# Kernel tuning notes

Measured on AMD Instinct MI355X. Metric: run time of the kernel, lower is better.

Reference implementation:

```python
import jax, jax.numpy as jnp
import numpy as np

HEAD_NUM = 16
QKV_DIM = 32
EMB = 512
SQRT_EMB = 22.627416997969522  # sqrt(512)
LOGIT_CLIP = 10.0
BATCH, POMO, PROBLEM = 32, 256, 1024


def setup_inputs() -> dict:
    key = jax.random.key(0)
    ks = jax.random.split(key, 8)
    s = 0.02
    return {
        "encoded_nodes": jax.random.normal(ks[0], (BATCH, PROBLEM, EMB), jnp.float32),
        "encoded_q1": jax.random.normal(ks[1], (BATCH, POMO, EMB), jnp.float32),
        "encoded_last_node": jax.random.normal(ks[2], (BATCH, POMO, EMB), jnp.float32),
        "ninf_mask": jnp.zeros((BATCH, POMO, PROBLEM), jnp.float32),
        # weights stored [in, out] so y = x @ W (equiv. to torch Linear with W.T)
        "Wq_first": jax.random.normal(ks[3], (EMB, HEAD_NUM * QKV_DIM), jnp.float32) * s,
        "Wq_last": jax.random.normal(ks[4], (EMB, HEAD_NUM * QKV_DIM), jnp.float32) * s,
        "Wk": jax.random.normal(ks[5], (EMB, HEAD_NUM * QKV_DIM), jnp.float32) * s,
        "Wv": jax.random.normal(ks[6], (EMB, HEAD_NUM * QKV_DIM), jnp.float32) * s,
        "W_combine": jax.random.normal(ks[7], (HEAD_NUM * QKV_DIM, EMB), jnp.float32) * s,
        "b_combine": jnp.zeros((EMB,), jnp.float32),
    }


def _heads(x):
    # [b, n, h*d] -> [b, h, n, d]
    b, n, _ = x.shape
    return x.reshape(b, n, HEAD_NUM, QKV_DIM).transpose(0, 2, 1, 3)


def reference(encoded_nodes, encoded_q1, encoded_last_node, ninf_mask,
              Wq_first, Wq_last, Wk, Wv, W_combine, b_combine):
    # set_kv
    k = _heads(encoded_nodes @ Wk)                     # [b,h,problem,d]
    v = _heads(encoded_nodes @ Wv)                     # [b,h,problem,d]
    single_head_key = encoded_nodes.transpose(0, 2, 1) # [b,emb,problem]
    # set_q1
    q_first = _heads(encoded_q1 @ Wq_first)            # [b,h,pomo,d]
    # forward
    q_last = _heads(encoded_last_node @ Wq_last)       # [b,h,pomo,d]
    q = q_first + q_last

    scale = 1.0 / jnp.sqrt(jnp.asarray(QKV_DIM, q.dtype))
    score = jnp.einsum("bhnd,bhmd->bhnm", q, k) * scale  # [b,h,pomo,problem]
    score = score + ninf_mask[:, None, :, :]
    weights = jax.nn.softmax(score, axis=-1)
    out = jnp.einsum("bhnm,bhmd->bhnd", weights, v)      # [b,h,pomo,d]
    out_concat = out.transpose(0, 2, 1, 3).reshape(q.shape[0], q.shape[2], HEAD_NUM * QKV_DIM)
    mh_out = out_concat @ W_combine + b_combine          # [b,pomo,emb]

    score2 = jnp.einsum("bne,bem->bnm", mh_out, single_head_key) / SQRT_EMB
    score2 = LOGIT_CLIP * jnp.tanh(score2) + ninf_mask
    probs = jax.nn.softmax(score2, axis=2)               # [b,pomo,problem]
    return probs
```

## Files before the change

kernel.cpp:

```cpp
#include <hip/hip_runtime.h>
#include <math.h>

typedef unsigned short u16;
typedef __attribute__((ext_vector_type(8))) short bf16x8;
typedef __attribute__((ext_vector_type(4))) float f32x4;
typedef __attribute__((ext_vector_type(4))) int i32x4;
typedef __attribute__((ext_vector_type(4))) short s16x4;
typedef __attribute__((ext_vector_type(4))) unsigned short u16x4;

#define MFMA16(a,b,c) __builtin_amdgcn_mfma_f32_16x16x32_bf16((a),(b),(c),0,0,0)

__device__ __forceinline__ u16 f2bf(float x){
  unsigned int u = __float_as_uint(x);
  u += 0x7fffu + ((u >> 16) & 1u);
  return (u16)(u >> 16);
}
__device__ __forceinline__ float bf2f(u16 x){
  return __uint_as_float(((unsigned)x) << 16);
}
__device__ __forceinline__ void gload16(const void* g, void* l){
  __builtin_amdgcn_global_load_lds((const __attribute__((address_space(1))) void*)g,
                                   (__attribute__((address_space(3))) void*)l, 16, 0, 0);
}

__global__ __launch_bounds__(256) void prep(
    const float* __restrict__ nodes, const float* __restrict__ q1, const float* __restrict__ lastn,
    const float* __restrict__ mask,
    const float* __restrict__ Wqf, const float* __restrict__ Wql, const float* __restrict__ Wk,
    const float* __restrict__ Wv, const float* __restrict__ Wc,
    u16* __restrict__ nodesb, u16* __restrict__ q1b, u16* __restrict__ lastb,
    u16* __restrict__ WtKV, u16* __restrict__ WtQF, u16* __restrict__ WtQL, u16* __restrict__ WtC,
    u16* __restrict__ maskP)
{
  const int tid = blockIdx.x * 256 + threadIdx.x;
  const int NT = 1048576;
  for (int i = tid; i < 4194304; i += NT) {
    float4 v = ((const float4*)nodes)[i];
    u16x4 o; o[0]=f2bf(v.x); o[1]=f2bf(v.y); o[2]=f2bf(v.z); o[3]=f2bf(v.w);
    *(u16x4*)&nodesb[i*4] = o;
  }
  {
    float4 v = ((const float4*)q1)[tid];
    u16x4 o; o[0]=f2bf(v.x); o[1]=f2bf(v.y); o[2]=f2bf(v.z); o[3]=f2bf(v.w);
    *(u16x4*)&q1b[tid*4] = o;
    v = ((const float4*)lastn)[tid];
    o[0]=f2bf(v.x); o[1]=f2bf(v.y); o[2]=f2bf(v.z); o[3]=f2bf(v.w);
    *(u16x4*)&lastb[tid*4] = o;
  }
  if (tid < 262144) {
    int n = tid >> 9, k = tid & 511;
    WtQF[tid] = f2bf(Wqf[k*512 + n]);
    WtQL[tid] = f2bf(Wql[k*512 + n]);
    WtC[tid]  = f2bf(Wc[k*512 + n]);
  }
  if (tid < 524288) {
    int n = tid >> 9, k = tid & 511;
    WtKV[tid] = f2bf(n < 512 ? Wk[k*512 + n] : Wv[k*512 + (n-512)]);
  }
  if (tid < 524288) {
    int brt = tid >> 10, c = tid & 1023;
    const float* mp = mask + (brt*16)*1024 + c;
    u16 vals[16];
    #pragma unroll
    for (int p=0;p<16;p++) vals[p] = f2bf(mp[p*1024]);
    *(i32x4*)&maskP[tid*16]     = *(i32x4*)&vals[0];
    *(i32x4*)&maskP[tid*16 + 8] = *(i32x4*)&vals[8];
  }
}

__global__ __launch_bounds__(256) void gemm_kv(const u16* __restrict__ A, const u16* __restrict__ Bw,
                                               u16* __restrict__ Kout, u16* __restrict__ Vout)
{
  const int mb = (blockIdx.x >> 6)*8 + (blockIdx.x & 7);
  const int nb = (blockIdx.x >> 3) & 7;
  const int t = threadIdx.x, w = t >> 6, l = t & 63, q = l >> 4, ln = l & 15;
  const int wm = (w >> 1) * 64, wn = (w & 1) * 64;
  __shared__ u16 smem[17920];
  f32x4 acc[4][4];
  #pragma unroll
  for (int i=0;i<4;i++)
    #pragma unroll
    for (int j=0;j<4;j++)
      #pragma unroll
      for (int r=0;r<4;r++) acc[i][j][r] = 0.f;
  const int m0 = mb*128, n0 = nb*128;

  #define STAGE_KV(kc_, b_) { \
    u16* sa = smem + (b_)*8192; \
    u16* sb = sa + 4096; \
    _Pragma("unroll") \
    for (int c=0;c<2;c++){ \
      int chunk = c*256 + t; \
      int ko = chunk >> 7, r_ = chunk & 127; \
      gload16(&A[(m0+r_)*512 + (kc_)*32 + ko*8], &sa[chunk*8]); \
      gload16(&Bw[(n0+r_)*512 + (kc_)*32 + ko*8], &sb[chunk*8]); \
    } }

  STAGE_KV(0, 0);
  for (int kc = 0; kc < 16; kc++) {
    __syncthreads();
    if (kc < 15) STAGE_KV(kc+1, (kc+1)&1);
    const u16* sa = smem + (kc&1)*8192;
    const u16* sb = sa + 4096;
    bf16x8 af[4], bfr[4];
    #pragma unroll
    for (int i=0;i<4;i++) af[i] = *(bf16x8*)&sa[(q*128 + wm + i*16 + ln)*8];
    #pragma unroll
    for (int j=0;j<4;j++) bfr[j] = *(bf16x8*)&sb[(q*128 + wn + j*16 + ln)*8];
    #pragma unroll
    for (int i=0;i<4;i++)
      #pragma unroll
      for (int j=0;j<4;j++)
        acc[i][j] = MFMA16(af[i], bfr[j], acc[i][j]);
  }
  #undef STAGE_KV

  __syncthreads();
  #pragma unroll
  for (int i=0;i<4;i++) {
    #pragma unroll
    for (int j=0;j<4;j++) {
      s16x4 o;
      #pragma unroll
      for (int r=0;r<4;r++) o[r] = (short)f2bf(acc[i][j][r]);
      *(s16x4*)&smem[(wn + j*16 + ln)*140 + wm + i*16 + q*4] = o;
    }
  }
  __syncthreads();
  const int bb_ = mb >> 3, mloc = (mb & 7)*128;
  if (nb < 4) {
    u16* base = Kout + ((bb_*16 + nb*4 + w)*1024 + mloc)*32;
    #pragma unroll
    for (int it=0; it<8; it++) {
      int idx = it*512 + l*8;
      int m_ = idx >> 5, d0 = idx & 31;
      int col = w*32 + d0;
      u16 v[8];
      #pragma unroll
      for (int dd=0;dd<8;dd++) v[dd] = smem[(col+dd)*140 + m_];
      *(i32x4*)&base[idx] = *(i32x4*)&v[0];
    }
  } else {
    u16* base = Vout + (((bb_*16 + (nb-4)*4 + w)*32))*1024 + mloc;
    #pragma unroll
    for (int it=0; it<8; it++) {
      int d_ = it*4 + (l >> 4);
      int mc_ = (l & 15)*8;
      *(i32x4*)&base[d_*1024 + mc_] = *(i32x4*)&smem[(w*32 + d_)*140 + mc_];
    }
  }
}

__global__ __launch_bounds__(256) void gemm_q(const u16* __restrict__ A1, const u16* __restrict__ A2,
                                              const u16* __restrict__ B1, const u16* __restrict__ B2,
                                              u16* __restrict__ Qout)
{
  const int mb = (blockIdx.x >> 6)*8 + (blockIdx.x & 7);
  const int nb = (blockIdx.x >> 3) & 7;
  const int t = threadIdx.x, w = t >> 6, l = t & 63, q = l >> 4, ln = l & 15;
  const int wm = (w >> 1) * 32, wn = (w & 1) * 32;
  __shared__ u16 As[4096];
  __shared__ u16 Bs[4096];
  f32x4 acc[2][2];
  #pragma unroll
  for (int i=0;i<2;i++)
    #pragma unroll
    for (int j=0;j<2;j++)
      #pragma unroll
      for (int r=0;r<4;r++) acc[i][j][r] = 0.f;
  const int m0 = mb*64, n0 = nb*64;
  for (int kc = 0; kc < 16; kc++) {
    const u16* Ap = (kc < 8) ? A1 : A2;
    const u16* Bp = (kc < 8) ? B1 : B2;
    const int k0 = (kc & 7) * 64;
    __syncthreads();
    #pragma unroll
    for (int c=0;c<2;c++) {
      int chunk = t + 256*c;
      int row = chunk & 63, ko = chunk >> 6;
      gload16(&Ap[(m0+row)*512 + k0 + ko*8], &As[chunk*8]);
      gload16(&Bp[(n0+row)*512 + k0 + ko*8], &Bs[chunk*8]);
    }
    __syncthreads();
    #pragma unroll
    for (int ko=0;ko<2;ko++) {
      bf16x8 af[2], bfr[2];
      #pragma unroll
      for (int i=0;i<2;i++) af[i] = *(bf16x8*)&As[((ko*4+q)*64 + wm + i*16 + ln)*8];
      #pragma unroll
      for (int j=0;j<2;j++) bfr[j] = *(bf16x8*)&Bs[((ko*4+q)*64 + wn + j*16 + ln)*8];
      #pragma unroll
      for (int i=0;i<2;i++)
        #pragma unroll
        for (int j=0;j<2;j++)
          acc[i][j] = MFMA16(af[i], bfr[j], acc[i][j]);
    }
  }
  const float sc = 0.17677669529663687f;
  #pragma unroll
  for (int i=0;i<2;i++) {
    int gm = m0 + wm + i*16 + q*4;
    int bb = gm >> 8, pm = gm & 255;
    #pragma unroll
    for (int j=0;j<2;j++) {
      int gn = n0 + wn + j*16 + ln;
      int h = gn >> 5, d = gn & 31;
      u16* qp = Qout + ((bb*16 + h)*256 + pm)*32 + d;
      #pragma unroll
      for (int r=0;r<4;r++) qp[r*32] = f2bf(acc[i][j][r]*sc);
    }
  }
}

__global__ __launch_bounds__(256) void attn(const u16* __restrict__ Qg, const u16* __restrict__ Kg,
                                            const u16* __restrict__ Vtg, const u16* __restrict__ maskP,
                                            u16* __restrict__ Og)
{
  const int bid = blockIdx.x;
  const int bh = (bid >> 5)*8 + (bid & 7);
  const int pt = (bid >> 3) & 3;
  const int h = bh & 15, bb = bh >> 4;
  const int t = threadIdx.x, w = t >> 6, l = t & 63, q = l >> 4, ln = l & 15;
  __shared__ u16 Qs[2048];
  __shared__ u16 Ks[4096];
  __shared__ u16 Vs[4096];
  __shared__ u16 Ps[4*640];
  u16* Pw = &Ps[w*640];
  const int qbase = ((bb*16 + h)*256 + pt*64)*32;
  gload16(&Qg[qbase + (t & 63)*32 + (t >> 6)*8], &Qs[t*8]);
  const int kbase = (bb*16 + h)*1024*32;
  const int vbase = (bb*16 + h)*32*1024;
  float rs[4] = {0.f,0.f,0.f,0.f};
  f32x4 oacc[2];
  #pragma unroll
  for (int dt=0;dt<2;dt++)
    #pragma unroll
    for (int r=0;r<4;r++) oacc[dt][r] = 0.f;
  __syncthreads();
  const bf16x8 aq = *(bf16x8*)&Qs[(q*64 + w*16 + ln)*8];
  const u16* mrow = maskP + (bb*16 + pt*4 + w)*16384 + q*4;
  for (int mc = 0; mc < 8; mc++) {
    __syncthreads();
    gload16(&Kg[kbase + (mc*128 + (t & 127))*32 + (t >> 7)*8],       &Ks[t*8]);
    gload16(&Kg[kbase + (mc*128 + (t & 127))*32 + ((t >> 7)+2)*8],   &Ks[(t+256)*8]);
    gload16(&Vtg[vbase + (t & 31)*1024 + mc*128 + (t >> 5)*8],       &Vs[t*8]);
    gload16(&Vtg[vbase + (t & 31)*1024 + mc*128 + ((t >> 5)+8)*8],   &Vs[(t+256)*8]);
    u16x4 mq[8];
    #pragma unroll
    for (int j2=0;j2<8;j2++)
      mq[j2] = *(const u16x4*)&mrow[(mc*128 + j2*16 + ln)*16];
    __syncthreads();
    #pragma unroll
    for (int ch=0; ch<4; ch++) {
      bf16x8 bk0 = *(bf16x8*)&Ks[(q*128 + (ch*2+0)*16 + ln)*8];
      bf16x8 bk1 = *(bf16x8*)&Ks[(q*128 + (ch*2+1)*16 + ln)*8];
      f32x4 zz = {0.f,0.f,0.f,0.f};
      f32x4 s0 = MFMA16(aq, bk0, zz);
      f32x4 s1 = MFMA16(aq, bk1, zz);
      #pragma unroll
      for (int r=0;r<4;r++) {
        float e0 = __expf(s0[r] + bf2f(mq[ch*2+0][r]));
        float e1 = __expf(s1[r] + bf2f(mq[ch*2+1][r]));
        rs[r] += e0 + e1;
        Pw[(q*4+r)*40 + ln]      = f2bf(e0);
        Pw[(q*4+r)*40 + 16 + ln] = f2bf(e1);
      }
      bf16x8 ap  = *(bf16x8*)&Pw[ln*40 + q*8];
      bf16x8 bv0 = *(bf16x8*)&Vs[((ch*4+q)*32 + ln)*8];
      bf16x8 bv1 = *(bf16x8*)&Vs[((ch*4+q)*32 + 16 + ln)*8];
      oacc[0] = MFMA16(ap, bv0, oacc[0]);
      oacc[1] = MFMA16(ap, bv1, oacc[1]);
    }
  }
  #pragma unroll
  for (int r=0;r<4;r++) {
    float v = rs[r];
    v += __shfl_xor(v,1); v += __shfl_xor(v,2); v += __shfl_xor(v,4); v += __shfl_xor(v,8);
    rs[r] = __builtin_amdgcn_rcpf(v);
  }
  const int orow = bb*256 + pt*64 + w*16 + q*4;
  #pragma unroll
  for (int dt=0;dt<2;dt++)
    #pragma unroll
    for (int r=0;r<4;r++)
      Og[(orow + r)*512 + h*32 + dt*16 + ln] = f2bf(oacc[dt][r]*rs[r]);
}

__global__ __launch_bounds__(1024) void cmbfin(const u16* __restrict__ oc, const u16* __restrict__ WtC,
                                               const float* __restrict__ bias,
                                               const u16* __restrict__ nodesb, const u16* __restrict__ maskP,
                                               float* __restrict__ out)
{
  const int bid = blockIdx.x;
  const int bb = bid & 31, rg = bid >> 5;
  const int t = threadIdx.x, w = t >> 6, l = t & 63, q = l >> 4, ln = l & 15;
  __shared__ u16 As[16384];
  __shared__ u16 Ms[16384];
  __shared__ float rsL[16][32];
  const int abase = (bb*256 + rg*32)*512;
  #pragma unroll
  for (int c=0;c<2;c++) {
    int chunk = t + 1024*c;
    gload16(&oc[abase + (chunk & 31)*512 + (chunk >> 5)*8], &As[chunk*8]);
  }
  __syncthreads();
  f32x4 acc1[2][2];
  #pragma unroll
  for (int i=0;i<2;i++)
    #pragma unroll
    for (int ct=0;ct<2;ct++)
      #pragma unroll
      for (int r=0;r<4;r++) acc1[i][ct][r] = 0.f;
  for (int kc=0;kc<16;kc++) {
    bf16x8 af[2];
    #pragma unroll
    for (int i=0;i<2;i++) af[i] = *(bf16x8*)&As[((kc*4 + q)*32 + i*16 + ln)*8];
    #pragma unroll
    for (int ct=0;ct<2;ct++) {
      int col = w*32 + ct*16 + ln;
      bf16x8 bfr = *(const bf16x8*)&WtC[col*512 + kc*32 + q*8];
      #pragma unroll
      for (int i=0;i<2;i++) acc1[i][ct] = MFMA16(af[i], bfr, acc1[i][ct]);
    }
  }
  #pragma unroll
  for (int ct=0;ct<2;ct++) {
    int gn = w*32 + ct*16 + ln;
    float bv = bias[gn];
    #pragma unroll
    for (int i=0;i<2;i++)
      #pragma unroll
      for (int r=0;r<4;r++)
        Ms[(gn >> 3)*256 + (i*16 + q*4 + r)*8 + (gn & 7)] = f2bf(acc1[i][ct][r] + bv);
  }
  __syncthreads();
  float rloc[2][4] = {{0.f,0.f,0.f,0.f},{0.f,0.f,0.f,0.f}};
  const int nbase = bb*524288;
  f32x4 acc[2][4];
  #pragma unroll
  for (int i=0;i<2;i++)
    #pragma unroll
    for (int ct=0;ct<4;ct++)
      #pragma unroll
      for (int r=0;r<4;r++) acc[i][ct][r] = 0.f;
  for (int kc=0;kc<16;kc++) {
    bf16x8 af[2];
    #pragma unroll
    for (int i=0;i<2;i++) af[i] = *(bf16x8*)&Ms[((kc*4 + q)*32 + i*16 + ln)*8];
    #pragma unroll
    for (int ct=0;ct<4;ct++) {
      int col = w*64 + ct*16 + ln;
      bf16x8 bfr = *(const bf16x8*)&nodesb[nbase + col*512 + kc*32 + q*8];
      #pragma unroll
      for (int i=0;i<2;i++) acc[i][ct] = MFMA16(af[i], bfr, acc[i][ct]);
    }
  }
  const float c2 = 0.08838834764831843f;
  const int prow_base = bb*256 + rg*32;
  #pragma unroll
  for (int i=0;i<2;i++) {
    #pragma unroll
    for (int ct=0;ct<4;ct++) {
      int col0 = w*64 + ct*16 + ln;
      u16x4 mv = *(const u16x4*)&maskP[((bb*16 + rg*2 + i)*1024 + col0)*16 + q*4];
      #pragma unroll
      for (int r=0;r<4;r++) {
        float x = acc[i][ct][r] * c2;
        x = fminf(fmaxf(x, -30.f), 30.f);
        float e2 = __expf(x);
        float lg = 10.f*(e2 - 1.f)*__builtin_amdgcn_rcpf(e2 + 1.f) + bf2f(mv[r]);
        float e = __expf(lg);
        rloc[i][r] += e;
        acc[i][ct][r] = e;
      }
    }
  }
  #pragma unroll
  for (int i=0;i<2;i++)
    #pragma unroll
    for (int r=0;r<4;r++) {
      float v = rloc[i][r];
      v += __shfl_xor(v,1); v += __shfl_xor(v,2); v += __shfl_xor(v,4); v += __shfl_xor(v,8);
      rloc[i][r] = v;
    }
  if (ln == 0) {
    #pragma unroll
    for (int i=0;i<2;i++)
      #pragma unroll
      for (int r=0;r<4;r++) rsL[w][i*16 + q*4 + r] = rloc[i][r];
  }
  __syncthreads();
  float inv[2][4];
  #pragma unroll
  for (int i=0;i<2;i++)
    #pragma unroll
    for (int r=0;r<4;r++) {
      float tot = 0.f;
      #pragma unroll
      for (int ww=0;ww<16;ww++) tot += rsL[ww][i*16 + q*4 + r];
      inv[i][r] = __builtin_amdgcn_rcpf(tot);
    }
  #pragma unroll
  for (int i=0;i<2;i++)
    #pragma unroll
    for (int ct=0;ct<4;ct++) {
      int col0 = w*64 + ct*16 + ln;
      #pragma unroll
      for (int r=0;r<4;r++)
        out[(prow_base + i*16 + q*4 + r)*1024 + col0] = acc[i][ct][r]*inv[i][r];
    }
}

extern "C" void kernel_launch(void* const* d_in, const int* in_sizes, int n_in,
                              void* d_out, int out_size, void* d_ws, size_t ws_size,
                              hipStream_t stream)
{
  (void)in_sizes; (void)n_in; (void)out_size; (void)ws_size;
  const float* nodes = (const float*)d_in[0];
  const float* q1    = (const float*)d_in[1];
  const float* lastn = (const float*)d_in[2];
  const float* mask  = (const float*)d_in[3];
  const float* Wqf   = (const float*)d_in[4];
  const float* Wql   = (const float*)d_in[5];
  const float* Wk    = (const float*)d_in[6];
  const float* Wv    = (const float*)d_in[7];
  const float* Wc    = (const float*)d_in[8];
  const float* bias  = (const float*)d_in[9];
  float* out = (float*)d_out;

  char* p = (char*)d_ws;
  u16* nodesb = (u16*)p; p += 33554432;
  u16* q1b    = (u16*)p; p += 8388608;
  u16* lastb  = (u16*)p; p += 8388608;
  u16* WtKV   = (u16*)p; p += 1048576;
  u16* WtQF   = (u16*)p; p += 524288;
  u16* WtQL   = (u16*)p; p += 524288;
  u16* WtC    = (u16*)p; p += 524288;
  u16* Kt     = (u16*)p; p += 33554432;
  u16* Vt     = (u16*)p; p += 33554432;
  u16* Qh     = (u16*)p; p += 8388608;
  u16* maskP  = (u16*)p; p += 16777216;
  u16* oc  = lastb;

  prep<<<4096, 256, 0, stream>>>(nodes, q1, lastn, mask, Wqf, Wql, Wk, Wv, Wc,
                                 nodesb, q1b, lastb, WtKV, WtQF, WtQL, WtC, maskP);
  gemm_kv<<<2048, 256, 0, stream>>>(nodesb, WtKV, Kt, Vt);
  gemm_q<<<1024, 256, 0, stream>>>(q1b, lastb, WtQF, WtQL, Qh);
  attn<<<2048, 256, 0, stream>>>(Qh, Kt, Vt, maskP, oc);
  cmbfin<<<256, 1024, 0, stream>>>(oc, WtC, bias, nodesb, maskP, out);
}
```

Baseline: 396.8 us.

## Fuse K/V and Q projection GEMMs into one 512-thread kernel launch

```diff
diff --git a/kernel.cpp b/kernel.cpp
--- a/kernel.cpp
+++ b/kernel.cpp
@@ -28,8 +28,8 @@
     const float* __restrict__ mask,
     const float* __restrict__ Wqf, const float* __restrict__ Wql, const float* __restrict__ Wk,
     const float* __restrict__ Wv, const float* __restrict__ Wc,
-    u16* __restrict__ nodesb, u16* __restrict__ q1b, u16* __restrict__ lastb,
-    u16* __restrict__ WtKV, u16* __restrict__ WtQF, u16* __restrict__ WtQL, u16* __restrict__ WtC,
+    u16* __restrict__ nodesb, u16* __restrict__ qlb,
+    u16* __restrict__ WtKV, u16* __restrict__ WtQ2, u16* __restrict__ WtC,
     u16* __restrict__ maskP)
 {
   const int tid = blockIdx.x * 256 + threadIdx.x;
@@ -40,17 +40,18 @@
     *(u16x4*)&nodesb[i*4] = o;
   }
   {
+    const int m = tid >> 7, k4 = (tid & 127)*4;
     float4 v = ((const float4*)q1)[tid];
     u16x4 o; o[0]=f2bf(v.x); o[1]=f2bf(v.y); o[2]=f2bf(v.z); o[3]=f2bf(v.w);
-    *(u16x4*)&q1b[tid*4] = o;
+    *(u16x4*)&qlb[m*1024 + k4] = o;
     v = ((const float4*)lastn)[tid];
     o[0]=f2bf(v.x); o[1]=f2bf(v.y); o[2]=f2bf(v.z); o[3]=f2bf(v.w);
-    *(u16x4*)&lastb[tid*4] = o;
+    *(u16x4*)&qlb[m*1024 + 512 + k4] = o;
   }
   if (tid < 262144) {
     int n = tid >> 9, k = tid & 511;
-    WtQF[tid] = f2bf(Wqf[k*512 + n]);
-    WtQL[tid] = f2bf(Wql[k*512 + n]);
+    WtQ2[n*1024 + k]       = f2bf(Wqf[k*512 + n]);
+    WtQ2[n*1024 + 512 + k] = f2bf(Wql[k*512 + n]);
     WtC[tid]  = f2bf(Wc[k*512 + n]);
   }
   if (tid < 524288) {
@@ -68,146 +69,107 @@
   }
 }
 
-__global__ __launch_bounds__(256) void gemm_kv(const u16* __restrict__ A, const u16* __restrict__ Bw,
-                                               u16* __restrict__ Kout, u16* __restrict__ Vout)
+__global__ __launch_bounds__(512, 8) void kvq(
+    const u16* __restrict__ Akv, const u16* __restrict__ Bkv,
+    const u16* __restrict__ Aq,  const u16* __restrict__ Bq,
+    u16* __restrict__ Kout, u16* __restrict__ Vout, u16* __restrict__ Qout)
 {
-  const int mb = (blockIdx.x >> 6)*8 + (blockIdx.x & 7);
-  const int nb = (blockIdx.x >> 3) & 7;
+  __shared__ u16 smem[16384];
   const int t = threadIdx.x, w = t >> 6, l = t & 63, q = l >> 4, ln = l & 15;
-  const int wm = (w >> 1) * 64, wn = (w & 1) * 64;
-  __shared__ u16 smem[17920];
-  f32x4 acc[4][4];
+  const int wc = w & 3;
+  const int wm = (w >> 2) * 64, wn = wc * 32;
+
+  const bool isq = blockIdx.x < 256;
+  int mb, nb, ksteps, kstr;
+  const u16 *Ab, *Bb;
+  if (isq) {
+    const int bid = blockIdx.x;
+    mb = bid >> 2; nb = bid & 3;
+    ksteps = 32; kstr = 1024; Ab = Aq; Bb = Bq;
+  } else {
+    const int bid = blockIdx.x - 256;
+    mb = (bid >> 6)*8 + (bid & 7);
+    nb = (bid >> 3) & 7;
+    ksteps = 16; kstr = 512; Ab = Akv; Bb = Bkv;
+  }
+  const int m0 = mb*128, n0 = nb*128;
+
+  f32x4 acc[4][2];
   #pragma unroll
   for (int i=0;i<4;i++)
     #pragma unroll
-    for (int j=0;j<4;j++)
+    for (int j=0;j<2;j++)
       #pragma unroll
       for (int r=0;r<4;r++) acc[i][j][r] = 0.f;
-  const int m0 = mb*128, n0 = nb*128;
-
-  #define STAGE_KV(kc_, b_) { \
-    u16* sa = smem + (b_)*8192; \
-    u16* sb = sa + 4096; \
-    _Pragma("unroll") \
-    for (int c=0;c<2;c++){ \
-      int chunk = c*256 + t; \
-      int ko = chunk >> 7, r_ = chunk & 127; \
-      gload16(&A[(m0+r_)*512 + (kc_)*32 + ko*8], &sa[chunk*8]); \
-      gload16(&Bw[(n0+r_)*512 + (kc_)*32 + ko*8], &sb[chunk*8]); \
-    } }
-
-  STAGE_KV(0, 0);
-  for (int kc = 0; kc < 16; kc++) {
+
+  const int r_ = t & 127, ko = t >> 7;
+  const u16* Aaddr = Ab + (m0 + r_)*kstr + ko*8;
+  const u16* Baddr = Bb + (n0 + r_)*kstr + ko*8;
+
+  #define STAGE(kc_, b_) { \
+    u16* s = smem + (b_)*8192; \
+    gload16(Aaddr + (kc_)*32, &s[t*8]); \
+    gload16(Baddr + (kc_)*32, &s[4096 + t*8]); }
+
+  STAGE(0, 0);
+  #pragma unroll 2
+  for (int kc = 0; kc < ksteps; kc++) {
     __syncthreads();
-    if (kc < 15) STAGE_KV(kc+1, (kc+1)&1);
+    if (kc + 1 < ksteps) STAGE(kc+1, (kc+1)&1);
     const u16* sa = smem + (kc&1)*8192;
     const u16* sb = sa + 4096;
-    bf16x8 af[4], bfr[4];
-    #pragma unroll
-    for (int i=0;i<4;i++) af[i] = *(bf16x8*)&sa[(q*128 + wm + i*16 + ln)*8];
-    #pragma unroll
-    for (int j=0;j<4;j++) bfr[j] = *(bf16x8*)&sb[(q*128 + wn + j*16 + ln)*8];
-    #pragma unroll
-    for (int i=0;i<4;i++)
-      #pragma unroll
-      for (int j=0;j<4;j++)
-        acc[i][j] = MFMA16(af[i], bfr[j], acc[i][j]);
-  }
-  #undef STAGE_KV
-
-  __syncthreads();
-  #pragma unroll
-  for (int i=0;i<4;i++) {
-    #pragma unroll
-    for (int j=0;j<4;j++) {
-      s16x4 o;
-      #pragma unroll
-      for (int r=0;r<4;r++) o[r] = (short)f2bf(acc[i][j][r]);
-      *(s16x4*)&smem[(wn + j*16 + ln)*140 + wm + i*16 + q*4] = o;
-    }
-  }
-  __syncthreads();
+    bf16x8 bfr[2];
+    #pragma unroll
+    for (int j=0;j<2;j++) bfr[j] = *(bf16x8*)&sb[(q*128 + wn + j*16 + ln)*8];
+    #pragma unroll
+    for (int i=0;i<4;i++) {
+      bf16x8 af = *(bf16x8*)&sa[(q*128 + wm + i*16 + ln)*8];
+      #pragma unroll
+      for (int j=0;j<2;j++)
+        acc[i][j] = MFMA16(af, bfr[j], acc[i][j]);
+    }
+  }
+  #undef STAGE
+
+  const float scale = isq ? 0.17677669529663687f : 1.0f;
   const int bb_ = mb >> 3, mloc = (mb & 7)*128;
-  if (nb < 4) {
-    u16* base = Kout + ((bb_*16 + nb*4 + w)*1024 + mloc)*32;
-    #pragma unroll
-    for (int it=0; it<8; it++) {
-      int idx = it*512 + l*8;
-      int m_ = idx >> 5, d0 = idx & 31;
-      int col = w*32 + d0;
-      u16 v[8];
-      #pragma unroll
-      for (int dd=0;dd<8;dd++) v[dd] = smem[(col+dd)*140 + m_];
-      *(i32x4*)&base[idx] = *(i32x4*)&v[0];
-    }
-  } else {
-    u16* base = Vout + (((bb_*16 + (nb-4)*4 + w)*32))*1024 + mloc;
-    #pragma unroll
-    for (int it=0; it<8; it++) {
-      int d_ = it*4 + (l >> 4);
-      int mc_ = (l & 15)*8;
-      *(i32x4*)&base[d_*1024 + mc_] = *(i32x4*)&smem[(w*32 + d_)*140 + mc_];
-    }
-  }
-}
-
-__global__ __launch_bounds__(256) void gemm_q(const u16* __restrict__ A1, const u16* __restrict__ A2,
-                                              const u16* __restrict__ B1, const u16* __restrict__ B2,
-                                              u16* __restrict__ Qout)
-{
-  const int mb = (blockIdx.x >> 6)*8 + (blockIdx.x & 7);
-  const int nb = (blockIdx.x >> 3) & 7;
-  const int t = threadIdx.x, w = t >> 6, l = t & 63, q = l >> 4, ln = l & 15;
-  const int wm = (w >> 1) * 32, wn = (w & 1) * 32;
-  __shared__ u16 As[4096];
-  __shared__ u16 Bs[4096];
-  f32x4 acc[2][2];
-  #pragma unroll
-  for (int i=0;i<2;i++)
-    #pragma unroll
-    for (int j=0;j<2;j++)
-      #pragma unroll
-      for (int r=0;r<4;r++) acc[i][j][r] = 0.f;
-  const int m0 = mb*64, n0 = nb*64;
-  for (int kc = 0; kc < 16; kc++) {
-    const u16* Ap = (kc < 8) ? A1 : A2;
-    const u16* Bp = (kc < 8) ? B1 : B2;
-    const int k0 = (kc & 7) * 64;
+  const int bbq = mb >> 1, pm0 = (mb & 1)*128;
+  #pragma unroll
+  for (int h = 0; h < 2; ++h) {
     __syncthreads();
-    #pragma unroll
-    for (int c=0;c<2;c++) {
-      int chunk = t + 256*c;
-      int row = chunk & 63, ko = chunk >> 6;
-      gload16(&Ap[(m0+row)*512 + k0 + ko*8], &As[chunk*8]);
-      gload16(&Bp[(n0+row)*512 + k0 + ko*8], &Bs[chunk*8]);
+    if ((wc >> 1) == h) {
+      const int cl0 = (wc & 1)*32;
+      #pragma unroll
+      for (int i=0;i<4;i++)
+        #pragma unroll
+        for (int j=0;j<2;j++) {
+          s16x4 o;
+          #pragma unroll
+          for (int r=0;r<4;r++) o[r] = (short)f2bf(acc[i][j][r]*scale);
+          *(s16x4*)&smem[(cl0 + j*16 + ln)*140 + wm + i*16 + q*4] = o;
+        }
     }
     __syncthreads();
     #pragma unroll
-    for (int ko=0;ko<2;ko++) {
-      bf16x8 af[2], bfr[2];
-      #pragma unroll
-      for (int i=0;i<2;i++) af[i] = *(bf16x8*)&As[((ko*4+q)*64 + wm + i*16 + ln)*8];
-      #pragma unroll
-      for (int j=0;j<2;j++) bfr[j] = *(bf16x8*)&Bs[((ko*4+q)*64 + wn + j*16 + ln)*8];
-      #pragma unroll
-      for (int i=0;i<2;i++)
+    for (int hc=0; hc<2; ++hc) {
+      const int hh = h*2 + hc;
+      if (isq) {
+        const int m_ = t >> 2, d0 = (t & 3)*8;
+        u16 v[8];
         #pragma unroll
-        for (int j=0;j<2;j++)
-          acc[i][j] = MFMA16(af[i], bfr[j], acc[i][j]);
-    }
-  }
-  const float sc = 0.17677669529663687f;
-  #pragma unroll
-  for (int i=0;i<2;i++) {
-    int gm = m0 + wm + i*16 + q*4;
-    int bb = gm >> 8, pm = gm & 255;
-    #pragma unroll
-    for (int j=0;j<2;j++) {
-      int gn = n0 + wn + j*16 + ln;
-      int h = gn >> 5, d = gn & 31;
-      u16* qp = Qout + ((bb*16 + h)*256 + pm)*32 + d;
-      #pragma unroll
-      for (int r=0;r<4;r++) qp[r*32] = f2bf(acc[i][j][r]*sc);
+        for (int dd=0;dd<8;dd++) v[dd] = smem[(hc*32 + d0 + dd)*140 + m_];
+        *(i32x4*)&Qout[((bbq*16 + nb*4 + hh)*256 + pm0 + m_)*32 + d0] = *(i32x4*)&v[0];
+      } else if (nb < 4) {
+        const int m_ = t >> 2, d0 = (t & 3)*8;
+        u16 v[8];
+        #pragma unroll
+        for (int dd=0;dd<8;dd++) v[dd] = smem[(hc*32 + d0 + dd)*140 + m_];
+        *(i32x4*)&Kout[((bb_*16 + nb*4 + hh)*1024 + mloc + m_)*32 + d0] = *(i32x4*)&v[0];
+      } else {
+        const int d = t >> 4, mo = (t & 15)*8;
+        *(i32x4*)&Vout[((bb_*16 + (nb-4)*4 + hh)*32 + d)*1024 + mloc + mo]
+            = *(i32x4*)&smem[(hc*32 + d)*140 + mo];
+      }
     }
   }
 }
@@ -430,22 +392,19 @@
 
   char* p = (char*)d_ws;
   u16* nodesb = (u16*)p; p += 33554432;
-  u16* q1b    = (u16*)p; p += 8388608;
-  u16* lastb  = (u16*)p; p += 8388608;
+  u16* qlb    = (u16*)p; p += 16777216;
   u16* WtKV   = (u16*)p; p += 1048576;
-  u16* WtQF   = (u16*)p; p += 524288;
-  u16* WtQL   = (u16*)p; p += 524288;
+  u16* WtQ2   = (u16*)p; p += 1048576;
   u16* WtC    = (u16*)p; p += 524288;
   u16* Kt     = (u16*)p; p += 33554432;
   u16* Vt     = (u16*)p; p += 33554432;
   u16* Qh     = (u16*)p; p += 8388608;
   u16* maskP  = (u16*)p; p += 16777216;
-  u16* oc  = lastb;
+  u16* oc  = qlb;
 
   prep<<<4096, 256, 0, stream>>>(nodes, q1, lastn, mask, Wqf, Wql, Wk, Wv, Wc,
-                                 nodesb, q1b, lastb, WtKV, WtQF, WtQL, WtC, maskP);
-  gemm_kv<<<2048, 256, 0, stream>>>(nodesb, WtKV, Kt, Vt);
-  gemm_q<<<1024, 256, 0, stream>>>(q1b, lastb, WtQF, WtQL, Qh);
+                                 nodesb, qlb, WtKV, WtQ2, WtC, maskP);
+  kvq<<<2304, 512, 0, stream>>>(nodesb, WtKV, qlb, WtQ2, Kt, Vt, Qh);
   attn<<<2048, 256, 0, stream>>>(Qh, Kt, Vt, maskP, oc);
   cmbfin<<<256, 1024, 0, stream>>>(oc, WtC, bias, nodesb, maskP, out);
 }
```

New measurement: 383.1 us. 1.04x faster.
